# Kernel tuning notes

Measured on AMD Instinct MI355X. Metric: run time of the kernel, lower is better.

Reference implementation:

```python
import jax, jax.numpy as jnp
import numpy as np


def _log_g(x):
    # log of g(x) = where(x>=0, x+0.5, sigmoid(x)), computed stably in log-space
    return jnp.where(x >= 0, jnp.log(jax.nn.relu(x) + 0.5), -jax.nn.softplus(-x))


def _mingru_layer(h, w_hg_l, w_out_l, rms_w_l):
    # h: [B,T,H]; w_hg_l: [2*DI,H]; w_out_l: [H,DI]; rms_w_l: [H]
    hg = jnp.einsum('bth,dh->btd', h, w_hg_l)          # [B,T,2*DI]
    hidden, gate = jnp.split(hg, 2, axis=-1)            # each [B,T,DI]
    log_coeffs = -jax.nn.softplus(gate)                 # log a_t
    log_values = -jax.nn.softplus(-gate) + _log_g(hidden)  # log(z_t * g(h~_t))
    # Heinsen log-space associative scan (prev_hidden = 0, contributes nothing)
    a_star = jnp.cumsum(log_coeffs, axis=1)
    log_h = a_star + jax.lax.cumlogsumexp(log_values - a_star, axis=1)
    out = jnp.exp(log_h)                                # [B,T,DI]
    out = jnp.einsum('btd,hd->bth', out, w_out_l) + h   # proj_out + residual
    eps = jnp.finfo(out.dtype).eps
    out = out * jax.lax.rsqrt(jnp.mean(out * out, axis=-1, keepdims=True) + eps)
    return out * rms_w_l


def setup_inputs() -> dict:
    key = jax.random.key(0)
    ks = jax.random.split(key, 6)
    B, T, OBS, H, DI, L, A = 32, 1024, 512, 512, 1024, 2, 16
    s = 0.05  # weight scale keeps softplus/exp chain well-conditioned
    return {
        'x': jax.random.normal(ks[0], (B, T, OBS), jnp.float32),
        'enc_w': s * jax.random.normal(ks[1], (H, OBS), jnp.float32),
        'enc_b': jnp.zeros((H,), jnp.float32),
        'w_hg': s * jax.random.normal(ks[2], (L, 2 * DI, H), jnp.float32),
        'w_out': s * jax.random.normal(ks[3], (L, H, DI), jnp.float32),
        'rms_w': jnp.ones((L, H), jnp.float32),
        'dec_w': s * jax.random.normal(ks[4], (A, H), jnp.float32),
        'dec_b': jnp.zeros((A,), jnp.float32),
        'val_w': s * jax.random.normal(ks[5], (1, H), jnp.float32),
        'val_b': jnp.zeros((1,), jnp.float32),
    }


def reference(x, enc_w, enc_b, w_hg, w_out, rms_w, dec_w, dec_b, val_w, val_b):
    B, T, _ = x.shape
    # encoder: Linear + exact gelu
    h = jax.nn.gelu(jnp.einsum('bto,ho->bth', x, enc_w) + enc_b, approximate=False)
    for l in range(w_hg.shape[0]):
        h = _mingru_layer(h, w_hg[l], w_out[l], rms_w[l])
    flat = h.reshape(B * T, -1)
    logits = flat @ dec_w.T + dec_b                     # [B*T, A]
    values = (flat @ val_w.T + val_b).reshape(B, T)
    return logits, values
```

## Files before the change

### kernel.cpp

```cpp
#include <hip/hip_runtime.h>
#include <math.h>

#define MROWS 32768
#define T_LEN 1024

typedef __attribute__((ext_vector_type(8))) short bf16x8;
typedef __attribute__((ext_vector_type(4))) float f32x4;

__device__ __forceinline__ unsigned short f2bf(float f) {
  union { float f; unsigned u; } x; x.f = f;
  unsigned r = x.u + 0x7fffu + ((x.u >> 16) & 1u);
  return (unsigned short)(r >> 16);
}
__device__ __forceinline__ float bf2f(unsigned short u) {
  union { unsigned u; float f; } x; x.u = ((unsigned)u) << 16; return x.f;
}

__device__ __forceinline__ void gload_lds16(const void* g, void* l) {
  __builtin_amdgcn_global_load_lds(
      (const __attribute__((address_space(1))) void*)g,
      (__attribute__((address_space(3))) void*)l, 16, 0, 0);
}

__device__ __forceinline__ float sigm_neg(float x) {
  return __builtin_amdgcn_rcpf(1.0f + __expf(x));
}

template<int MODE>
__global__ __launch_bounds__(256, 2)
void gemm_bt(const unsigned short* __restrict__ A, int lda,
             const unsigned short* __restrict__ B,
             int N, int K,
             const float* __restrict__ bias,
             const unsigned short* res,
             unsigned short* outb)
{
  __shared__ __align__(16) unsigned short sA[128 * 64];
  __shared__ __align__(16) unsigned short sB[128 * 64];
  const int tid  = threadIdx.x;
  const int wave = tid >> 6, lane = tid & 63;
  const int m0 = blockIdx.y * 128, n0 = blockIdx.x * 128;
  const int srow   = lane >> 3;
  const int sslotb = ((lane & 7) ^ srow) * 16;
  const int wm = wave & 1, wn = wave >> 1;
  const int r16 = lane & 15, q = lane >> 4;

  f32x4 acc[4][4];
#pragma unroll
  for (int i = 0; i < 4; i++)
#pragma unroll
    for (int j = 0; j < 4; j++)
#pragma unroll
      for (int e = 0; e < 4; e++) acc[i][j][e] = 0.0f;

  const char* Ab = (const char*)A;
  const char* Bb = (const char*)B;
  char* sAb = (char*)sA;
  char* sBb = (char*)sB;

  for (int kt = 0; kt < K; kt += 64) {
#pragma unroll
    for (int i = 0; i < 4; i++) {
      const int j = wave * 4 + i;
      const int row = j * 8 + srow;
      gload_lds16(Ab + ((size_t)(m0 + row) * lda + kt) * 2 + sslotb, sAb + j * 1024);
      gload_lds16(Bb + ((size_t)(n0 + row) * K   + kt) * 2 + sslotb, sBb + j * 1024);
    }
    __syncthreads();
#pragma unroll
    for (int kh = 0; kh < 2; kh++) {
      bf16x8 af[4], bfr[4];
#pragma unroll
      for (int mt = 0; mt < 4; mt++) {
        const int row = wm * 64 + mt * 16 + r16;
        af[mt] = *(const bf16x8*)(sAb + row * 128 + ((((kh << 2) | q) ^ (row & 7)) * 16));
      }
#pragma unroll
      for (int nt = 0; nt < 4; nt++) {
        const int row = wn * 64 + nt * 16 + r16;
        bfr[nt] = *(const bf16x8*)(sBb + row * 128 + ((((kh << 2) | q) ^ (row & 7)) * 16));
      }
#pragma unroll
      for (int mt = 0; mt < 4; mt++)
#pragma unroll
        for (int nt = 0; nt < 4; nt++)
          acc[mt][nt] = __builtin_amdgcn_mfma_f32_16x16x32_bf16(af[mt], bfr[nt], acc[mt][nt], 0, 0, 0);
    }
    __syncthreads();
  }

  const bool isgate = (MODE == 3) && (n0 >= 1024);
#pragma unroll
  for (int mt = 0; mt < 4; mt++) {
#pragma unroll
    for (int nt = 0; nt < 4; nt++) {
#pragma unroll
      for (int r = 0; r < 4; r++) {
        const int m = m0 + wm * 64 + mt * 16 + q * 4 + r;
        const int n = n0 + wn * 64 + nt * 16 + r16;
        const size_t idx = (size_t)m * N + n;
        float v = acc[mt][nt][r];
        if (MODE == 0) {
          v += bias[n];
          v = 0.5f * v * (1.0f + erff(v * 0.70710678118654752f));
        } else if (MODE == 2) {
          v += bf2f(res[idx]);
        } else if (MODE == 3) {
          if (isgate) {
            v = sigm_neg(v);
          } else {
            v = (v >= 0.0f) ? (v + 0.5f) : sigm_neg(-v);
          }
        }
        outb[idx] = f2bf(v);
      }
    }
  }
}

__global__ __launch_bounds__(256)
void scan_kernel(unsigned short* hg) {
  __shared__ unsigned long long sAB[256 * 16];
  __shared__ float sA[16 * 32];
  __shared__ float sH[16 * 32];
  const int b  = blockIdx.x >> 5;
  const int dg = blockIdx.x & 31;
  const int tid = threadIdx.x;
  const int c  = tid >> 4;
  const int dp = tid & 15;
  unsigned int* base = (unsigned int*)(hg + (size_t)b * T_LEN * 2048);
  const int du = dg * 16 + dp;

  float carry = 0.0f;

  for (int seg = 0; seg < 4; ++seg) {
    const int t0 = seg * 256 + c * 16;

    float A0 = 1.0f, A1 = 1.0f, h0 = 0.0f, h1 = 0.0f;
#pragma unroll
    for (int tl = 0; tl < 16; ++tl) {
      const int t = t0 + tl;
      const unsigned Gp  = base[t * 1024 + du];
      const unsigned apk = base[t * 1024 + 512 + du];
      const float G0  = bf2f((unsigned short)Gp),  G1  = bf2f((unsigned short)(Gp >> 16));
      const float fa0 = bf2f((unsigned short)apk), fa1 = bf2f((unsigned short)(apk >> 16));
      const unsigned short rb0 = f2bf((1.0f - fa0) * G0);
      const unsigned short rb1 = f2bf((1.0f - fa1) * G1);
      sAB[(c * 16 + tl) * 16 + dp] =
          (unsigned long long)apk |
          ((unsigned long long)((unsigned)rb0 | ((unsigned)rb1 << 16)) << 32);
      const float fb0 = bf2f(rb0), fb1 = bf2f(rb1);
      A0 *= fa0; h0 = fa0 * h0 + fb0;
      A1 *= fa1; h1 = fa1 * h1 + fb1;
    }
    sA[c * 32 + 2 * dp] = A0;  sA[c * 32 + 2 * dp + 1] = A1;
    sH[c * 32 + 2 * dp] = h0;  sH[c * 32 + 2 * dp + 1] = h1;
    __syncthreads();

    if (tid < 32) {
      float hin = carry;
#pragma unroll
      for (int cc = 0; cc < 16; ++cc) {
        const float a  = sA[cc * 32 + tid];
        const float hs = sH[cc * 32 + tid];
        sA[cc * 32 + tid] = hin;
        hin = hs + a * hin;
      }
      carry = hin;
    }
    __syncthreads();

    float hh0 = sA[c * 32 + 2 * dp];
    float hh1 = sA[c * 32 + 2 * dp + 1];
#pragma unroll
    for (int tl = 0; tl < 16; ++tl) {
      const int t = t0 + tl;
      const unsigned long long ab = sAB[(c * 16 + tl) * 16 + dp];
      const float fa0 = bf2f((unsigned short)ab);
      const float fa1 = bf2f((unsigned short)(ab >> 16));
      const float fb0 = bf2f((unsigned short)(ab >> 32));
      const float fb1 = bf2f((unsigned short)(ab >> 48));
      hh0 = fa0 * hh0 + fb0;
      hh1 = fa1 * hh1 + fb1;
      base[t * 1024 + 512 + du] = (unsigned)f2bf(hh0) | ((unsigned)f2bf(hh1) << 16);
    }
    __syncthreads();
  }
}

__global__ __launch_bounds__(256)
void rms_kernel(unsigned short* __restrict__ hb, const float* __restrict__ w) {
  const int wid  = (blockIdx.x * blockDim.x + threadIdx.x) >> 6;
  const int lane = threadIdx.x & 63;
  unsigned short* row = hb + (size_t)wid * 512;
  float v[8];
  float ss = 0.0f;
#pragma unroll
  for (int j = 0; j < 8; j++) { v[j] = bf2f(row[lane + 64 * j]); ss += v[j] * v[j]; }
#pragma unroll
  for (int off = 32; off >= 1; off >>= 1) ss += __shfl_xor(ss, off, 64);
  const float r = rsqrtf(ss * (1.0f / 512.0f) + 1.1920929e-7f);
#pragma unroll
  for (int j = 0; j < 8; j++) {
    const int k = lane + 64 * j;
    row[k] = f2bf(v[j] * r * w[k]);
  }
}

__global__ __launch_bounds__(256)
void decoder_kernel(const unsigned short* __restrict__ hb,
                    const float* __restrict__ dec_w,
                    const float* __restrict__ dec_b,
                    const float* __restrict__ val_w,
                    const float* __restrict__ val_b,
                    float* __restrict__ out) {
  const int nw   = (gridDim.x * blockDim.x) >> 6;
  const int wid  = (blockIdx.x * blockDim.x + threadIdx.x) >> 6;
  const int lane = threadIdx.x & 63;
  float* logits = out;
  float* values = out + (size_t)MROWS * 16;
  for (int row = wid; row < MROWS; row += nw) {
    const unsigned short* hr = hb + (size_t)row * 512;
    float acc[17];
#pragma unroll
    for (int a = 0; a < 17; a++) acc[a] = 0.0f;
#pragma unroll
    for (int j = 0; j < 8; j++) {
      const int k = lane + 64 * j;
      const float hv = bf2f(hr[k]);
#pragma unroll
      for (int a = 0; a < 16; a++) acc[a] += hv * dec_w[a * 512 + k];
      acc[16] += hv * val_w[k];
    }
#pragma unroll
    for (int a = 0; a < 17; a++) {
#pragma unroll
      for (int off = 32; off >= 1; off >>= 1) acc[a] += __shfl_xor(acc[a], off, 64);
    }
    if (lane == 0) {
#pragma unroll
      for (int a = 0; a < 16; a++) logits[(size_t)row * 16 + a] = acc[a] + dec_b[a];
      values[row] = acc[16] + val_b[0];
    }
  }
}

__global__ __launch_bounds__(256)
void conv_bf16(const float* __restrict__ in, unsigned short* __restrict__ out, int n4) {
  const int i = blockIdx.x * blockDim.x + threadIdx.x;
  if (i < n4) {
    const float4 v = ((const float4*)in)[i];
    const unsigned long long pack =
        (unsigned long long)f2bf(v.x) |
        ((unsigned long long)f2bf(v.y) << 16) |
        ((unsigned long long)f2bf(v.z) << 32) |
        ((unsigned long long)f2bf(v.w) << 48);
    ((unsigned long long*)out)[i] = pack;
  }
}

extern "C" void kernel_launch(void* const* d_in, const int* in_sizes, int n_in,
                              void* d_out, int out_size, void* d_ws, size_t ws_size,
                              hipStream_t stream) {
  const float* x     = (const float*)d_in[0];
  const float* enc_w = (const float*)d_in[1];
  const float* enc_b = (const float*)d_in[2];
  const float* w_hg  = (const float*)d_in[3];
  const float* w_out = (const float*)d_in[4];
  const float* rms_w = (const float*)d_in[5];
  const float* dec_w = (const float*)d_in[6];
  const float* dec_b = (const float*)d_in[7];
  const float* val_w = (const float*)d_in[8];
  const float* val_b = (const float*)d_in[9];
  float* out = (float*)d_out;

  if (ws_size < 174587904u) return;

  char* ws = (char*)d_ws;
  unsigned short* hg   = (unsigned short*)(ws);
  unsigned short* xb   = (unsigned short*)(ws);
  unsigned short* hb   = (unsigned short*)(ws + 134217728);
  unsigned short* wenc = (unsigned short*)(ws + 167772160);
  unsigned short* whg  = wenc + 262144;
  unsigned short* wout = whg + 2097152;

  conv_bf16<<<16384, 256, 0, stream>>>(x, xb, 4194304);
  conv_bf16<<<256,   256, 0, stream>>>(enc_w, wenc, 65536);
  conv_bf16<<<2048,  256, 0, stream>>>(w_hg, whg, 524288);
  conv_bf16<<<1024,  256, 0, stream>>>(w_out, wout, 262144);

  gemm_bt<0><<<dim3(4, 256), 256, 0, stream>>>(xb, 512, wenc, 512, 512, enc_b, nullptr, hb);

  for (int l = 0; l < 2; ++l) {
    gemm_bt<3><<<dim3(16, 256), 256, 0, stream>>>(hb, 512, whg + (size_t)l * 1048576, 2048, 512,
                                                  nullptr, nullptr, hg);
    scan_kernel<<<1024, 256, 0, stream>>>(hg);
    gemm_bt<2><<<dim3(4, 256), 256, 0, stream>>>(hg + 1024, 2048, wout + (size_t)l * 524288,
                                                 512, 1024, nullptr, hb, hb);
    rms_kernel<<<8192, 256, 0, stream>>>(hb, rms_w + (size_t)l * 512);
  }

  decoder_kernel<<<512, 256, 0, stream>>>(hb, dec_w, dec_b, val_w, val_b, out);
}
```

Baseline: 628.8 us.

## Fuse hidden/gate GEMM pair with scan coefficient math, swizzle grids, fuse final RMS into decoder

Adds a dedicated hidden/gate GEMM that computes each matching hidden and gate column tile in one block with two accumulator sets. Its epilogue writes the scan coefficients a and b directly, so the scan kernel no longer recomputes (1-a)*G. Existing GEMMs now use a 1D grid with a grouped swizzle to improve L2 reuse. The last layer's RMS norm is fused into the decoder, which removes one full read/write pass over the hidden state. The doubled accumulators (32 f32x4) and three LDS tiles raise register and LDS pressure, which could lower occupancy.

```diff
diff --git a/kernel.cpp b/kernel.cpp
--- a/kernel.cpp
+++ b/kernel.cpp
@@ -39,7 +39,10 @@
   __shared__ __align__(16) unsigned short sB[128 * 64];
   const int tid  = threadIdx.x;
   const int wave = tid >> 6, lane = tid & 63;
-  const int m0 = blockIdx.y * 128, n0 = blockIdx.x * 128;
+  const int lid = blockIdx.x;
+  const int swz = (lid & 7) * ((int)gridDim.x >> 3) + (lid >> 3);
+  const int m0 = (swz >> 2) * 128;
+  const int n0 = (swz & 3) * 128;
   const int srow   = lane >> 3;
   const int sslotb = ((lane & 7) ^ srow) * 16;
   const int wm = wave & 1, wn = wave >> 1;
@@ -89,7 +92,6 @@
     __syncthreads();
   }
 
-  const bool isgate = (MODE == 3) && (n0 >= 1024);
 #pragma unroll
   for (int mt = 0; mt < 4; mt++) {
 #pragma unroll
@@ -105,14 +107,98 @@
           v = 0.5f * v * (1.0f + erff(v * 0.70710678118654752f));
         } else if (MODE == 2) {
           v += bf2f(res[idx]);
-        } else if (MODE == 3) {
-          if (isgate) {
-            v = sigm_neg(v);
-          } else {
-            v = (v >= 0.0f) ? (v + 0.5f) : sigm_neg(-v);
-          }
         }
         outb[idx] = f2bf(v);
+      }
+    }
+  }
+}
+
+__global__ __launch_bounds__(256, 2)
+void gemm_hg(const unsigned short* __restrict__ A,
+             const unsigned short* __restrict__ B,
+             unsigned short* __restrict__ outb)
+{
+  __shared__ __align__(16) unsigned short sA [128 * 64];
+  __shared__ __align__(16) unsigned short sB0[128 * 64];
+  __shared__ __align__(16) unsigned short sB1[128 * 64];
+  const int tid  = threadIdx.x;
+  const int wave = tid >> 6, lane = tid & 63;
+  const int lid = blockIdx.x;
+  const int swz = (lid & 7) * 256 + (lid >> 3);
+  const int m0  = (swz >> 3) * 128;
+  const int nh0 = (swz & 7) * 128;
+  const int srow   = lane >> 3;
+  const int sslotb = ((lane & 7) ^ srow) * 16;
+  const int wm = wave & 1, wn = wave >> 1;
+  const int r16 = lane & 15, q = lane >> 4;
+
+  f32x4 acc0[4][4], acc1[4][4];
+#pragma unroll
+  for (int i = 0; i < 4; i++)
+#pragma unroll
+    for (int j = 0; j < 4; j++)
+#pragma unroll
+      for (int e = 0; e < 4; e++) { acc0[i][j][e] = 0.0f; acc1[i][j][e] = 0.0f; }
+
+  const char* Ab = (const char*)A;
+  const char* Bb = (const char*)B;
+  char* sAb  = (char*)sA;
+  char* sB0b = (char*)sB0;
+  char* sB1b = (char*)sB1;
+
+  for (int kt = 0; kt < 512; kt += 64) {
+#pragma unroll
+    for (int i = 0; i < 4; i++) {
+      const int j = wave * 4 + i;
+      const int row = j * 8 + srow;
+      gload_lds16(Ab + ((size_t)(m0 + row) * 512 + kt) * 2 + sslotb, sAb + j * 1024);
+      gload_lds16(Bb + ((size_t)(nh0 + row) * 512 + kt) * 2 + sslotb, sB0b + j * 1024);
+      gload_lds16(Bb + ((size_t)(1024 + nh0 + row) * 512 + kt) * 2 + sslotb, sB1b + j * 1024);
+    }
+    __syncthreads();
+#pragma unroll
+    for (int kh = 0; kh < 2; kh++) {
+      bf16x8 af[4], b0r[4], b1r[4];
+#pragma unroll
+      for (int mt = 0; mt < 4; mt++) {
+        const int row = wm * 64 + mt * 16 + r16;
+        af[mt] = *(const bf16x8*)(sAb + row * 128 + ((((kh << 2) | q) ^ (row & 7)) * 16));
+      }
+#pragma unroll
+      for (int nt = 0; nt < 4; nt++) {
+        const int row = wn * 64 + nt * 16 + r16;
+        const int so  = ((((kh << 2) | q) ^ (row & 7)) * 16);
+        b0r[nt] = *(const bf16x8*)(sB0b + row * 128 + so);
+        b1r[nt] = *(const bf16x8*)(sB1b + row * 128 + so);
+      }
+#pragma unroll
+      for (int mt = 0; mt < 4; mt++)
+#pragma unroll
+        for (int nt = 0; nt < 4; nt++) {
+          acc0[mt][nt] = __builtin_amdgcn_mfma_f32_16x16x32_bf16(af[mt], b0r[nt], acc0[mt][nt], 0, 0, 0);
+          acc1[mt][nt] = __builtin_amdgcn_mfma_f32_16x16x32_bf16(af[mt], b1r[nt], acc1[mt][nt], 0, 0, 0);
+        }
+    }
+    __syncthreads();
+  }
+
+#pragma unroll
+  for (int mt = 0; mt < 4; mt++) {
+#pragma unroll
+    for (int nt = 0; nt < 4; nt++) {
+#pragma unroll
+      for (int r = 0; r < 4; r++) {
+        const int m  = m0 + wm * 64 + mt * 16 + q * 4 + r;
+        const int d  = nh0 + wn * 64 + nt * 16 + r16;
+        const float vh = acc0[mt][nt][r];
+        const float vg = acc1[mt][nt][r];
+        const float G = (vh >= 0.0f) ? (vh + 0.5f) : sigm_neg(-vh);
+        const float a = sigm_neg(vg);
+        const float b = (1.0f - a) * G;
+        const size_t base = (size_t)m * 2048 + d;
+        outb[base]        = f2bf(b);
+        outb[base + 1024] = f2bf(a);
       }
     }
   }
@@ -140,16 +226,12 @@
 #pragma unroll
     for (int tl = 0; tl < 16; ++tl) {
       const int t = t0 + tl;
-      const unsigned Gp  = base[t * 1024 + du];
+      const unsigned bpk = base[t * 1024 + du];
       const unsigned apk = base[t * 1024 + 512 + du];
-      const float G0  = bf2f((unsigned short)Gp),  G1  = bf2f((unsigned short)(Gp >> 16));
+      sAB[(c * 16 + tl) * 16 + dp] =
+          (unsigned long long)apk | ((unsigned long long)bpk << 32);
       const float fa0 = bf2f((unsigned short)apk), fa1 = bf2f((unsigned short)(apk >> 16));
-      const unsigned short rb0 = f2bf((1.0f - fa0) * G0);
-      const unsigned short rb1 = f2bf((1.0f - fa1) * G1);
-      sAB[(c * 16 + tl) * 16 + dp] =
-          (unsigned long long)apk |
-          ((unsigned long long)((unsigned)rb0 | ((unsigned)rb1 << 16)) << 32);
-      const float fb0 = bf2f(rb0), fb1 = bf2f(rb1);
+      const float fb0 = bf2f((unsigned short)bpk), fb1 = bf2f((unsigned short)(bpk >> 16));
       A0 *= fa0; h0 = fa0 * h0 + fb0;
       A1 *= fa1; h1 = fa1 * h1 + fb1;
     }
@@ -208,40 +290,46 @@
 }
 
 __global__ __launch_bounds__(256)
-void decoder_kernel(const unsigned short* __restrict__ hb,
+void rms_dec_kernel(const unsigned short* __restrict__ hb,
+                    const float* __restrict__ w,
                     const float* __restrict__ dec_w,
                     const float* __restrict__ dec_b,
                     const float* __restrict__ val_w,
                     const float* __restrict__ val_b,
                     float* __restrict__ out) {
-  const int nw   = (gridDim.x * blockDim.x) >> 6;
-  const int wid  = (blockIdx.x * blockDim.x + threadIdx.x) >> 6;
+  const int row  = (blockIdx.x * blockDim.x + threadIdx.x) >> 6;
   const int lane = threadIdx.x & 63;
-  float* logits = out;
-  float* values = out + (size_t)MROWS * 16;
-  for (int row = wid; row < MROWS; row += nw) {
-    const unsigned short* hr = hb + (size_t)row * 512;
-    float acc[17];
-#pragma unroll
-    for (int a = 0; a < 17; a++) acc[a] = 0.0f;
-#pragma unroll
-    for (int j = 0; j < 8; j++) {
-      const int k = lane + 64 * j;
-      const float hv = bf2f(hr[k]);
-#pragma unroll
-      for (int a = 0; a < 16; a++) acc[a] += hv * dec_w[a * 512 + k];
-      acc[16] += hv * val_w[k];
-    }
-#pragma unroll
-    for (int a = 0; a < 17; a++) {
-#pragma unroll
-      for (int off = 32; off >= 1; off >>= 1) acc[a] += __shfl_xor(acc[a], off, 64);
-    }
-    if (lane == 0) {
-#pragma unroll
-      for (int a = 0; a < 16; a++) logits[(size_t)row * 16 + a] = acc[a] + dec_b[a];
-      values[row] = acc[16] + val_b[0];
-    }
+  const unsigned short* hr = hb + (size_t)row * 512;
+  float v[8];
+  float ss = 0.0f;
+#pragma unroll
+  for (int j = 0; j < 8; j++) { v[j] = bf2f(hr[lane + 64 * j]); ss += v[j] * v[j]; }
+#pragma unroll
+  for (int off = 32; off >= 1; off >>= 1) ss += __shfl_xor(ss, off, 64);
+  const float r = rsqrtf(ss * (1.0f / 512.0f) + 1.1920929e-7f);
+
+  float acc[17];
+#pragma unroll
+  for (int a = 0; a < 17; a++) acc[a] = 0.0f;
+#pragma unroll
+  for (int j = 0; j < 8; j++) {
+    const int k = lane + 64 * j;
+    const float hv = v[j] * r * w[k];
+#pragma unroll
+    for (int a = 0; a < 16; a++) acc[a] += hv * dec_w[a * 512 + k];
+    acc[16] += hv * val_w[k];
+  }
+#pragma unroll
+  for (int a = 0; a < 17; a++) {
+#pragma unroll
+    for (int off = 32; off >= 1; off >>= 1) acc[a] += __shfl_xor(acc[a], off, 64);
+  }
+  if (lane == 0) {
+    float* logits = out;
+    float* values = out + (size_t)MROWS * 16;
+#pragma unroll
+    for (int a = 0; a < 16; a++) logits[(size_t)row * 16 + a] = acc[a] + dec_b[a];
+    values[row] = acc[16] + val_b[0];
   }
 }
 
@@ -289,16 +377,16 @@
   conv_bf16<<<2048,  256, 0, stream>>>(w_hg, whg, 524288);
   conv_bf16<<<1024,  256, 0, stream>>>(w_out, wout, 262144);
 
-  gemm_bt<0><<<dim3(4, 256), 256, 0, stream>>>(xb, 512, wenc, 512, 512, enc_b, nullptr, hb);
+  gemm_bt<0><<<1024, 256, 0, stream>>>(xb, 512, wenc, 512, 512, enc_b, nullptr, hb);
 
   for (int l = 0; l < 2; ++l) {
-    gemm_bt<3><<<dim3(16, 256), 256, 0, stream>>>(hb, 512, whg + (size_t)l * 1048576, 2048, 512,
-                                                  nullptr, nullptr, hg);
+    gemm_hg<<<2048, 256, 0, stream>>>(hb, whg + (size_t)l * 1048576, hg);
     scan_kernel<<<1024, 256, 0, stream>>>(hg);
-    gemm_bt<2><<<dim3(4, 256), 256, 0, stream>>>(hg + 1024, 2048, wout + (size_t)l * 524288,
-                                                 512, 1024, nullptr, hb, hb);
-    rms_kernel<<<8192, 256, 0, stream>>>(hb, rms_w + (size_t)l * 512);
-  }
-
-  decoder_kernel<<<512, 256, 0, stream>>>(hb, dec_w, dec_b, val_w, val_b, out);
-}
+    gemm_bt<2><<<1024, 256, 0, stream>>>(hg + 1024, 2048, wout + (size_t)l * 524288,
+                                         512, 1024, nullptr, hb, hb);
+    if (l == 0) rms_kernel<<<8192, 256, 0, stream>>>(hb, rms_w);
+  }
+
+  rms_dec_kernel<<<8192, 256, 0, stream>>>(hb, rms_w + 512, dec_w, dec_b,
+                                           val_w, val_b, out);
+}
```

Result: faster. 603.8 us (-4.0%).
